# Kernel tuning notes

Measured on AMD Instinct MI355X. Metric: run time of the kernel, lower is better.

Reference implementation:

```python
import jax, jax.numpy as jnp
import numpy as np

K = 5  # kernel_size, n_qubits = K*K = 25
PAD = (K - 1) // 2  # 'same' padding, stride 1


def _extract_patches(x):
    """x: [B, C, H, W] -> [B, C, H, W, K*K] 5x5 patches, zero 'same' padding."""
    B, C, H, W = x.shape
    xp = jnp.pad(x, ((0, 0), (0, 0), (PAD, PAD), (PAD, PAD)))
    # 25 static shifted views stacked on a trailing axis (fixed small loop)
    return jnp.stack(
        [xp[:, :, di:di + H, dj:dj + W] for di in range(K) for dj in range(K)],
        axis=-1,
    )


def _vqc_1mout(patches, w):
    """Analytic expectation <Z_0> of the vqc_1mout circuit:
    AngleEmbedding (RX) of the 25 patch values, one BasicEntanglerLayer
    (per-wire RX(w_i) followed by a CNOT ring 0->1->...->24->0), measure Z on
    wire 0. Heisenberg-propagating Z_0 through the CNOT ring gives the tensor
    product of Z on wires 1..24 over the product state after the RX rotations,
    so <Z_0> = prod_{i=1..24} cos(x_i + w_i).
    patches: [..., 25], w: [25] -> out: [...].
    """
    y = jnp.cos(patches + w)  # broadcast over trailing 25
    return jnp.prod(y[..., 1:], axis=-1)


def setup_inputs() -> dict:
    key = jax.random.key(0)
    kx, kw = jax.random.split(key)
    x = jax.random.normal(kx, (32, 16, 64, 64), dtype=jnp.float32)
    # learned VQC rotation angles (n_qlayers=1, 25 qubits)
    w = jax.random.uniform(kw, (K * K,), dtype=jnp.float32,
                           minval=0.0, maxval=2.0 * np.pi)
    return {"x": x, "w": w}


def reference(x, w):
    # depthwise quanvolution: out[b, f, h, w] = VQC(5x5 patch of x[b, f])
    patches = _extract_patches(x)          # [B, C, H, W, 25]
    return _vqc_1mout(patches, w)          # [B, C, H, W]
```

## Files before the change

kernel.cpp:

```cpp
#include <hip/hip_runtime.h>
#include <hip/hip_bf16.h>
#include <math.h>


#define TR   32
#define SMR  (TR + 4)
#define SMC  (64 + 4)

__device__ __forceinline__ float uni(float v) {
    return __uint_as_float(__builtin_amdgcn_readfirstlane(__float_as_uint(v)));
}

__global__ __launch_bounds__(256)
void qconv5x5_kernel(const float* __restrict__ x, const float* __restrict__ w,
                     float* __restrict__ out)
{
    __shared__ float2 sm[SMR][SMC];

    const int tid   = threadIdx.x;
    const int bid   = blockIdx.x;
    const int plane = bid >> 1;
    const int r0    = (bid & 1) * TR;

    float cw[25], sw[25];
#pragma unroll
    for (int p = 0; p < 25; ++p) {
        float s, c;
        __sincosf(w[p], &s, &c);
        cw[p] = uni(c);
        sw[p] = uni(s);
    }

    const float* xp = x + plane * 64 * 64;
    for (int i = tid; i < SMR * SMC; i += 256) {
        const int rr = i / SMC;
        const int cc = i - rr * SMC;
        const int gr = r0 + rr - 2;
        const int gc = cc - 2;
        float c = 1.0f, s = 0.0f;
        if ((unsigned)gr < 64u && (unsigned)gc < 64u) {
            __sincosf(xp[gr * 64 + gc], &s, &c);
        }
        sm[rr][cc] = make_float2(c, s);
    }
    __syncthreads();

    const int tx = tid & 63;
    const int q  = tid >> 6;

    float prod[8];
#pragma unroll
    for (int ro = 0; ro < 8; ++ro) prod[ro] = 1.0f;

#pragma unroll
    for (int nr = 0; nr < 12; ++nr) {
        const int tr = q * 8 + nr;
        float2 v[5];
#pragma unroll
        for (int dj = 0; dj < 5; ++dj) v[dj] = sm[tr][tx + dj];
#pragma unroll
        for (int ro = 0; ro < 8; ++ro) {
            const int di = nr - ro;
            if (di < 0 || di > 4) continue;
#pragma unroll
            for (int dj = 0; dj < 5; ++dj) {
                const int p = di * 5 + dj;
                if (p == 0) continue;
                prod[ro] *= fmaf(v[dj].x, cw[p], -(v[dj].y * sw[p]));
            }
        }
    }

    float* op = out + plane * 64 * 64 + (r0 + q * 8) * 64 + tx;
#pragma unroll
    for (int ro = 0; ro < 8; ++ro) op[ro * 64] = prod[ro];
}

extern "C" void kernel_launch(void* const* d_in, const int* in_sizes, int n_in,
                              void* d_out, int out_size, void* d_ws, size_t ws_size,
                              hipStream_t stream) {
    const float* x = (const float*)d_in[0];
    const float* w = (const float*)d_in[1];
    float* out = (float*)d_out;
    (void)in_sizes; (void)n_in; (void)out_size; (void)d_ws; (void)ws_size;

    const int planes = 32 * 16;
    dim3 grid(planes * (64 / TR));
    dim3 block(256);
    qconv5x5_kernel<<<grid, block, 0, stream>>>(x, w, out);
}
```

Measured before the change: 68.82 us.

## Remap threads to 2 columns x 4 rows with float4 LDS reads

Each thread now computes a 4-row by 2-column output tile instead of 8 rows by 1 column. Shared-memory rows are read as three float4 loads covering both neighbouring output columns, and results are stored as float2. The weight sin/cos is computed once per lane and broadcast with readlane instead of 25 sincos calls per thread. Per-output vertical reuse drops, since 8 rows are read for 4 outputs instead of 12 for 8, so total LDS traffic per output may shift, while the instruction count for the loads falls.

```diff
diff --git a/kernel.cpp b/kernel.cpp
--- a/kernel.cpp
+++ b/kernel.cpp
@@ -7,28 +7,29 @@
 #define SMR  (TR + 4)
 #define SMC  (64 + 4)
 
-__device__ __forceinline__ float uni(float v) {
-    return __uint_as_float(__builtin_amdgcn_readfirstlane(__float_as_uint(v)));
+__device__ __forceinline__ float rdlane(float v, int lane) {
+    return __uint_as_float(__builtin_amdgcn_readlane(__float_as_uint(v), lane));
 }
 
 __global__ __launch_bounds__(256)
 void qconv5x5_kernel(const float* __restrict__ x, const float* __restrict__ w,
                      float* __restrict__ out)
 {
-    __shared__ float2 sm[SMR][SMC];
+    __shared__ alignas(16) float2 sm[SMR][SMC];
 
     const int tid   = threadIdx.x;
     const int bid   = blockIdx.x;
     const int plane = bid >> 1;
     const int r0    = (bid & 1) * TR;
 
+    const int lane = tid & 63;
+    float sv, cv;
+    __sincosf(w[lane < 25 ? lane : 0], &sv, &cv);
     float cw[25], sw[25];
 #pragma unroll
     for (int p = 0; p < 25; ++p) {
-        float s, c;
-        __sincosf(w[p], &s, &c);
-        cw[p] = uni(c);
-        sw[p] = uni(s);
+        cw[p] = rdlane(cv, p);
+        sw[p] = rdlane(sv, p);
     }
 
     const float* xp = x + plane * 64 * 64;
@@ -45,35 +46,43 @@
     }
     __syncthreads();
 
-    const int tx = tid & 63;
-    const int q  = tid >> 6;
+    const int cp = tid & 31;
+    const int rq = tid >> 5;
 
-    float prod[8];
+    float prod[4][2];
 #pragma unroll
-    for (int ro = 0; ro < 8; ++ro) prod[ro] = 1.0f;
+    for (int ro = 0; ro < 4; ++ro) { prod[ro][0] = 1.f; prod[ro][1] = 1.f; }
 
 #pragma unroll
-    for (int nr = 0; nr < 12; ++nr) {
-        const int tr = q * 8 + nr;
-        float2 v[5];
+    for (int nr = 0; nr < 8; ++nr) {
+        const int tr = rq * 4 + nr;
+        const float4* rowp = reinterpret_cast<const float4*>(&sm[tr][0]);
+        float4 f0 = rowp[cp], f1 = rowp[cp + 1], f2 = rowp[cp + 2];
+        float2 arr6[6] = { make_float2(f0.x, f0.y), make_float2(f0.z, f0.w),
+                           make_float2(f1.x, f1.y), make_float2(f1.z, f1.w),
+                           make_float2(f2.x, f2.y), make_float2(f2.z, f2.w) };
 #pragma unroll
-        for (int dj = 0; dj < 5; ++dj) v[dj] = sm[tr][tx + dj];
-#pragma unroll
-        for (int ro = 0; ro < 8; ++ro) {
+        for (int ro = 0; ro < 4; ++ro) {
             const int di = nr - ro;
             if (di < 0 || di > 4) continue;
 #pragma unroll
             for (int dj = 0; dj < 5; ++dj) {
                 const int p = di * 5 + dj;
-                if (p == 0) continue;
-                prod[ro] *= fmaf(v[dj].x, cw[p], -(v[dj].y * sw[p]));
+#pragma unroll
+                for (int pa = 0; pa < 2; ++pa) {
+                    if (p == 0) continue;
+                    const float2 v = arr6[dj + pa];
+                    prod[ro][pa] *= fmaf(v.x, cw[p], -(v.y * sw[p]));
+                }
             }
         }
     }
 
-    float* op = out + plane * 64 * 64 + (r0 + q * 8) * 64 + tx;
+    float2* op = reinterpret_cast<float2*>(
+        out + plane * 64 * 64 + (r0 + rq * 4) * 64 + 2 * cp);
 #pragma unroll
-    for (int ro = 0; ro < 8; ++ro) op[ro * 64] = prod[ro];
+    for (int ro = 0; ro < 4; ++ro)
+        op[ro * 32] = make_float2(prod[ro][0], prod[ro][1]);
 }
 
 extern "C" void kernel_launch(void* const* d_in, const int* in_sizes, int n_in,
@@ -84,8 +93,7 @@
     float* out = (float*)d_out;
     (void)in_sizes; (void)n_in; (void)out_size; (void)d_ws; (void)ws_size;
 
-    const int planes = 32 * 16;
-    dim3 grid(planes * (64 / TR));
+    dim3 grid(512 * (64 / TR));
     dim3 block(256);
     qconv5x5_kernel<<<grid, block, 0, stream>>>(x, w, out);
 }
```

New measurement: 65.69 us. 4.5% less time.
